# Optimization experiments

Measured on AMD Instinct MI355X. Metric: run time of the kernel, lower is better.

## Reference

```python
import jax, jax.numpy as jnp
import numpy as np
import math

NUM_IN_C = 128      # rep_2d num_c (c_z)
ATT_C = 64          # attention_num_c
NUM_HEADS = 4
B, T, I, J = 1, 4, 256, 256


def setup_inputs() -> dict:
    key = jax.random.key(0)
    ks = jax.random.split(key, 7)
    s = 1.0 / math.sqrt(NUM_IN_C)
    return {
        "z2d": jax.random.normal(ks[0], (B, I, J, NUM_IN_C), dtype=jnp.float32),
        "t2d": jax.random.normal(ks[1], (B, T, I, J, NUM_IN_C), dtype=jnp.float32),
        # nn.Linear weights are [out_features, in_features]; apply as x @ W.T
        "Wq": jax.random.normal(ks[2], (ATT_C * NUM_HEADS, NUM_IN_C), dtype=jnp.float32) * s,
        "Wk": jax.random.normal(ks[3], (ATT_C * NUM_HEADS, NUM_IN_C), dtype=jnp.float32) * s,
        "Wv": jax.random.normal(ks[4], (ATT_C * NUM_HEADS, NUM_IN_C), dtype=jnp.float32) * s,
        "Wo": jax.random.normal(ks[5], (NUM_IN_C, ATT_C * NUM_HEADS), dtype=jnp.float32) * s,
        "bo": jax.random.normal(ks[6], (NUM_IN_C,), dtype=jnp.float32) * 0.02,
    }


def reference(z2d, t2d, Wq, Wk, Wv, Wo, bo):
    # Projections; reshape last dim to (attention_num_c, num_heads) per torch .view
    q = (z2d @ Wq.T).reshape(*z2d.shape[:-1], ATT_C, NUM_HEADS)        # b i j c h
    k = (t2d @ Wk.T).reshape(*t2d.shape[:-1], ATT_C, NUM_HEADS)        # b t i j c h
    v = (t2d @ Wv.T).reshape(*t2d.shape[:-1], ATT_C, NUM_HEADS)        # b t i j c h
    # NOTE: original scales by sqrt(num_in_c), not sqrt(attention_num_c)
    scores = jnp.einsum('bijch,btijch->btijh', q, k) / math.sqrt(NUM_IN_C)
    w = jax.nn.softmax(scores, axis=1)                                  # softmax over template axis t
    out = jnp.einsum('btijh,btijch->bijch', w, v)                       # b i j c h
    out = out.reshape(*out.shape[:-2], ATT_C * NUM_HEADS)               # flatten (c,h)
    return out @ Wo.T + bo
```

## Files before the change

kernel.cpp:

```cpp
#include <hip/hip_runtime.h>


#define PIX 65536

typedef __attribute__((ext_vector_type(8))) short s8v;
typedef __attribute__((ext_vector_type(4))) float f4v;
typedef __attribute__((ext_vector_type(4))) unsigned int u4v;
typedef __attribute__((ext_vector_type(4))) float fl4;

__device__ __forceinline__ unsigned short f2bf(float x) {
    unsigned int u = __float_as_uint(x);
    u = (u + 0x7FFFu + ((u >> 16) & 1u)) >> 16;
    return (unsigned short)u;
}

__device__ __forceinline__ unsigned int cvtpk(float lo, float hi) {
    unsigned int r;
    asm("v_cvt_pk_bf16_f32 %0, %1, %2" : "=v"(r) : "v"(lo), "v"(hi));
    return r;
}

__device__ __forceinline__ s8v pack8(fl4 d0, fl4 d1) {
    union { u4v u; s8v s; } cv;
    cv.u[0] = cvtpk(d0[0], d0[1]);
    cv.u[1] = cvtpk(d0[2], d0[3]);
    cv.u[2] = cvtpk(d1[0], d1[1]);
    cv.u[3] = cvtpk(d1[2], d1[3]);
    return cv.s;
}

__device__ __forceinline__ float bflo(unsigned int u) { return __uint_as_float(u << 16); }
__device__ __forceinline__ float bfhi(unsigned int u) { return __uint_as_float(u & 0xffff0000u); }

__global__ __launch_bounds__(256) void build_weights(
        const float* __restrict__ Wq, const float* __restrict__ Wk,
        const float* __restrict__ Wv, const float* __restrict__ Wo,
        unsigned short* __restrict__ mcat, unsigned short* __restrict__ pcat) {
    int b = blockIdx.x;
    if (b < 256) {
        int idx = b * 256 + threadIdx.x;
        int n = idx >> 7, k1 = idx & 127;
        int h = n >> 7, k2 = n & 127;
        float s = 0.f;
        #pragma unroll 8
        for (int c = 0; c < 64; c++) {
            int r = c * 4 + h;
            s += Wq[r * 128 + k1] * Wk[r * 128 + k2];
        }
        mcat[idx] = f2bf(s * 0.088388347648318447f);
    } else {
        int idx = (b - 256) * 256 + threadIdx.x;
        int m = idx >> 9, kk = idx & 511;
        int h = kk >> 7, k = kk & 127;
        float s = 0.f;
        #pragma unroll 8
        for (int c = 0; c < 64; c++) {
            int r = c * 4 + h;
            s += Wo[m * 256 + r] * Wv[r * 128 + k];
        }
        pcat[idx] = f2bf(s);
    }
}

__global__ __launch_bounds__(256, 3) void score_kernel(
    const float* __restrict__ z2d, const float* __restrict__ t2d,
    const unsigned short* __restrict__ mcat, float* __restrict__ wbuf) {

    __shared__ unsigned short sm[128 * 128];
    const int tid = threadIdx.x;
    const int wv = tid >> 6, lane = tid & 63, quad = lane >> 4, l15 = lane & 15;
    const int p = blockIdx.x * 64 + wv * 16 + l15;

    s8v za[4];
    {
        const float* zp = z2d + (size_t)p * 128 + quad * 8;
        #pragma unroll
        for (int ks = 0; ks < 4; ks++)
            za[ks] = pack8(*(const fl4*)(zp + ks * 32), *(const fl4*)(zp + ks * 32 + 4));
    }
    unsigned int a2[4][8][2];
    #pragma unroll
    for (int t = 0; t < 4; t++) {
        const float* ap = t2d + ((size_t)t * PIX + p) * 128 + quad * 4;
        #pragma unroll
        for (int cb = 0; cb < 8; cb++) {
            const fl4 v = *(const fl4*)(ap + cb * 16);
            a2[t][cb][0] = cvtpk(v[0], v[1]);
            a2[t][cb][1] = cvtpk(v[2], v[3]);
        }
    }

    for (int h = 0; h < 4; h++) {
        __syncthreads();
        #pragma unroll
        for (int i = 0; i < 8; i++) {
            const int g8 = i * 256 + tid;
            const int row = g8 >> 4, c8 = g8 & 15;
            *(u4v*)&sm[row * 128 + ((c8 ^ (row & 7)) * 8)] =
                *(const u4v*)(mcat + (size_t)(h * 128 + row) * 128 + c8 * 8);
        }
        __syncthreads();

        float ps[4] = {0.f, 0.f, 0.f, 0.f};
        #pragma unroll
        for (int cb = 0; cb < 8; cb++) {
            f4v u = {0.f, 0.f, 0.f, 0.f};
            #pragma unroll
            for (int ks = 0; ks < 4; ks++) {
                const s8v a = *(const s8v*)&sm[(cb * 16 + l15) * 128 +
                                               (((ks * 4 + quad) ^ (l15 & 7)) * 8)];
                u = __builtin_amdgcn_mfma_f32_16x16x32_bf16(a, za[ks], u, 0, 0, 0);
            }
            #pragma unroll
            for (int t = 0; t < 4; t++) {
                const float a0 = bflo(a2[t][cb][0]), a1 = bfhi(a2[t][cb][0]);
                const float b0 = bflo(a2[t][cb][1]), b1 = bfhi(a2[t][cb][1]);
                ps[t] += u[0] * a0 + u[1] * a1 + u[2] * b0 + u[3] * b1;
            }
        }
        #pragma unroll
        for (int t = 0; t < 4; t++) {
            ps[t] += __shfl_xor(ps[t], 16);
            ps[t] += __shfl_xor(ps[t], 32);
        }
        const float mx = fmaxf(fmaxf(ps[0], ps[1]), fmaxf(ps[2], ps[3]));
        float e[4], sum = 0.f;
        #pragma unroll
        for (int t = 0; t < 4; t++) { e[t] = __expf(ps[t] - mx); sum += e[t]; }
        const float inv = 1.f / sum;
        if (quad == 0) {
            #pragma unroll
            for (int t = 0; t < 4; t++)
                wbuf[(size_t)(h * 4 + t) * PIX + p] = e[t] * inv;
        }
    }
}

__global__ __launch_bounds__(256, 3) void out_kernel(
    const float* __restrict__ t2d, const unsigned short* __restrict__ pcat,
    const float* __restrict__ wbuf, const float* __restrict__ bo,
    float* __restrict__ out) {

    __shared__ unsigned short sm[128 * 128];
    const int tid = threadIdx.x;
    const int wv = tid >> 6, lane = tid & 63, quad = lane >> 4, l15 = lane & 15;
    const int p0 = blockIdx.x * 64 + wv * 16;
    const int p = p0 + l15;

    float wgt[4][4];
    #pragma unroll
    for (int h = 0; h < 4; h++)
        #pragma unroll
        for (int t = 0; t < 4; t++)
            wgt[h][t] = wbuf[(size_t)(h * 4 + t) * PIX + p];

    s8v af[4][4];
    #pragma unroll
    for (int kf = 0; kf < 4; kf++) {
        float f[4][8];
        #pragma unroll
        for (int h = 0; h < 4; h++)
            #pragma unroll
            for (int j = 0; j < 8; j++) f[h][j] = 0.f;
        #pragma unroll
        for (int t = 0; t < 4; t++) {
            const float* ap = t2d + ((size_t)t * PIX + p) * 128 + kf * 32 + quad * 8;
            const fl4 d0 = *(const fl4*)ap;
            const fl4 d1 = *(const fl4*)(ap + 4);
            #pragma unroll
            for (int h = 0; h < 4; h++) {
                const float w = wgt[h][t];
                #pragma unroll
                for (int j = 0; j < 4; j++) {
                    f[h][j]     += w * d0[j];
                    f[h][j + 4] += w * d1[j];
                }
            }
        }
        #pragma unroll
        for (int h = 0; h < 4; h++) {
            union { u4v u; s8v s; } cv;
            cv.u[0] = cvtpk(f[h][0], f[h][1]);
            cv.u[1] = cvtpk(f[h][2], f[h][3]);
            cv.u[2] = cvtpk(f[h][4], f[h][5]);
            cv.u[3] = cvtpk(f[h][6], f[h][7]);
            af[h][kf] = cv.s;
        }
    }

    f4v acc[8];
    #pragma unroll
    for (int ct = 0; ct < 8; ct++) acc[ct] = (f4v){0.f, 0.f, 0.f, 0.f};

    for (int h = 0; h < 4; h++) {
        __syncthreads();
        #pragma unroll
        for (int i = 0; i < 8; i++) {
            const int g8 = i * 256 + tid;
            const int row = g8 >> 4, c8 = g8 & 15;
            *(u4v*)&sm[row * 128 + ((c8 ^ (row & 7)) * 8)] =
                *(const u4v*)(pcat + (size_t)row * 512 + h * 128 + c8 * 8);
        }
        __syncthreads();
        #pragma unroll
        for (int kf = 0; kf < 4; kf++)
            #pragma unroll
            for (int ct = 0; ct < 8; ct++) {
                const s8v b = *(const s8v*)&sm[(ct * 16 + l15) * 128 +
                                               (((kf * 4 + quad) ^ (l15 & 7)) * 8)];
                acc[ct] = __builtin_amdgcn_mfma_f32_16x16x32_bf16(af[h][kf], b, acc[ct], 0, 0, 0);
            }
    }

    #pragma unroll
    for (int ct = 0; ct < 8; ct++) {
        const float bb = bo[ct * 16 + l15];
        #pragma unroll
        for (int r = 0; r < 4; r++)
            out[(size_t)(p0 + quad * 4 + r) * 128 + ct * 16 + l15] = acc[ct][r] + bb;
    }
}

extern "C" void kernel_launch(void* const* d_in, const int* in_sizes, int n_in,
                              void* d_out, int out_size, void* d_ws, size_t ws_size,
                              hipStream_t stream) {
    const float* z2d = (const float*)d_in[0];
    const float* t2d = (const float*)d_in[1];
    const float* Wq  = (const float*)d_in[2];
    const float* Wk  = (const float*)d_in[3];
    const float* Wv  = (const float*)d_in[4];
    const float* Wo  = (const float*)d_in[5];
    const float* bo  = (const float*)d_in[6];

    unsigned short* mcat = (unsigned short*)d_ws;
    unsigned short* pcat = mcat + 512 * 128;
    float* wbuf = (float*)(pcat + 128 * 512);

    build_weights<<<512, 256, 0, stream>>>(Wq, Wk, Wv, Wo, mcat, pcat);
    score_kernel<<<1024, 256, 0, stream>>>(z2d, t2d, mcat, wbuf);
    out_kernel<<<1024, 256, 0, stream>>>(t2d, pcat, wbuf, bo, (float*)d_out);
}
```

Baseline: 312.3 us.

## Drop LDS staging of fused weights; read MFMA operands directly from global/L2

Both score and output kernels stop copying the fused bf16 weight matrices into shared memory and instead load MFMA operands straight from global memory, relying on L1/L2 caching. This removes the LDS fill, the barriers and the shared-memory footprint, which may raise occupancy. Blocks are halved to 128 threads (2048 blocks), and the output kernel now interleaves the weighted template reduction with MFMA accumulation instead of buffering all A fragments. The cost is many more uncoalesced-ish global loads per wave, which could stress the vector memory path and caches.

```diff
diff --git a/kernel.cpp b/kernel.cpp
--- a/kernel.cpp
+++ b/kernel.cpp
@@ -62,14 +62,13 @@
     }
 }
 
-__global__ __launch_bounds__(256, 3) void score_kernel(
+__global__ __launch_bounds__(128, 4) void score_kernel(
     const float* __restrict__ z2d, const float* __restrict__ t2d,
     const unsigned short* __restrict__ mcat, float* __restrict__ wbuf) {
 
-    __shared__ unsigned short sm[128 * 128];
     const int tid = threadIdx.x;
     const int wv = tid >> 6, lane = tid & 63, quad = lane >> 4, l15 = lane & 15;
-    const int p = blockIdx.x * 64 + wv * 16 + l15;
+    const int p = blockIdx.x * 32 + wv * 16 + l15;
 
     s8v za[4];
     {
@@ -91,31 +90,21 @@
     }
 
     for (int h = 0; h < 4; h++) {
-        __syncthreads();
-        #pragma unroll
-        for (int i = 0; i < 8; i++) {
-            const int g8 = i * 256 + tid;
-            const int row = g8 >> 4, c8 = g8 & 15;
-            *(u4v*)&sm[row * 128 + ((c8 ^ (row & 7)) * 8)] =
-                *(const u4v*)(mcat + (size_t)(h * 128 + row) * 128 + c8 * 8);
-        }
-        __syncthreads();
-
+        const unsigned short* mh = mcat + (size_t)h * 128 * 128;
         float ps[4] = {0.f, 0.f, 0.f, 0.f};
         #pragma unroll
         for (int cb = 0; cb < 8; cb++) {
             f4v u = {0.f, 0.f, 0.f, 0.f};
             #pragma unroll
             for (int ks = 0; ks < 4; ks++) {
-                const s8v a = *(const s8v*)&sm[(cb * 16 + l15) * 128 +
-                                               (((ks * 4 + quad) ^ (l15 & 7)) * 8)];
+                const s8v a = *(const s8v*)(mh + (size_t)(cb * 16 + l15) * 128
+                                            + ks * 32 + quad * 8);
                 u = __builtin_amdgcn_mfma_f32_16x16x32_bf16(a, za[ks], u, 0, 0, 0);
             }
             #pragma unroll
             for (int t = 0; t < 4; t++) {
-                const float a0 = bflo(a2[t][cb][0]), a1 = bfhi(a2[t][cb][0]);
-                const float b0 = bflo(a2[t][cb][1]), b1 = bfhi(a2[t][cb][1]);
-                ps[t] += u[0] * a0 + u[1] * a1 + u[2] * b0 + u[3] * b1;
+                ps[t] += u[0] * bflo(a2[t][cb][0]) + u[1] * bfhi(a2[t][cb][0])
+                       + u[2] * bflo(a2[t][cb][1]) + u[3] * bfhi(a2[t][cb][1]);
             }
         }
         #pragma unroll
@@ -136,15 +125,14 @@
     }
 }
 
-__global__ __launch_bounds__(256, 3) void out_kernel(
+__global__ __launch_bounds__(128, 4) void out_kernel(
     const float* __restrict__ t2d, const unsigned short* __restrict__ pcat,
     const float* __restrict__ wbuf, const float* __restrict__ bo,
     float* __restrict__ out) {
 
-    __shared__ unsigned short sm[128 * 128];
     const int tid = threadIdx.x;
     const int wv = tid >> 6, lane = tid & 63, quad = lane >> 4, l15 = lane & 15;
-    const int p0 = blockIdx.x * 64 + wv * 16;
+    const int p0 = blockIdx.x * 32 + wv * 16;
     const int p = p0 + l15;
 
     float wgt[4][4];
@@ -154,8 +142,10 @@
         for (int t = 0; t < 4; t++)
             wgt[h][t] = wbuf[(size_t)(h * 4 + t) * PIX + p];
 
-    s8v af[4][4];
-    #pragma unroll
+    f4v acc[8];
+    #pragma unroll
+    for (int ct = 0; ct < 8; ct++) acc[ct] = (f4v){0.f, 0.f, 0.f, 0.f};
+
     for (int kf = 0; kf < 4; kf++) {
         float f[4][8];
         #pragma unroll
@@ -184,32 +174,14 @@
             cv.u[1] = cvtpk(f[h][2], f[h][3]);
             cv.u[2] = cvtpk(f[h][4], f[h][5]);
             cv.u[3] = cvtpk(f[h][6], f[h][7]);
-            af[h][kf] = cv.s;
-        }
-    }
-
-    f4v acc[8];
-    #pragma unroll
-    for (int ct = 0; ct < 8; ct++) acc[ct] = (f4v){0.f, 0.f, 0.f, 0.f};
-
-    for (int h = 0; h < 4; h++) {
-        __syncthreads();
-        #pragma unroll
-        for (int i = 0; i < 8; i++) {
-            const int g8 = i * 256 + tid;
-            const int row = g8 >> 4, c8 = g8 & 15;
-            *(u4v*)&sm[row * 128 + ((c8 ^ (row & 7)) * 8)] =
-                *(const u4v*)(pcat + (size_t)row * 512 + h * 128 + c8 * 8);
-        }
-        __syncthreads();
-        #pragma unroll
-        for (int kf = 0; kf < 4; kf++)
+            const s8v af = cv.s;
             #pragma unroll
             for (int ct = 0; ct < 8; ct++) {
-                const s8v b = *(const s8v*)&sm[(ct * 16 + l15) * 128 +
-                                               (((kf * 4 + quad) ^ (l15 & 7)) * 8)];
-                acc[ct] = __builtin_amdgcn_mfma_f32_16x16x32_bf16(af[h][kf], b, acc[ct], 0, 0, 0);
-            }
+                const s8v b = *(const s8v*)(pcat + (size_t)(ct * 16 + l15) * 512
+                                            + h * 128 + kf * 32 + quad * 8);
+                acc[ct] = __builtin_amdgcn_mfma_f32_16x16x32_bf16(af, b, acc[ct], 0, 0, 0);
+            }
+        }
     }
 
     #pragma unroll
@@ -237,6 +209,6 @@
     float* wbuf = (float*)(pcat + 128 * 512);
 
     build_weights<<<512, 256, 0, stream>>>(Wq, Wk, Wv, Wo, mcat, pcat);
-    score_kernel<<<1024, 256, 0, stream>>>(z2d, t2d, mcat, wbuf);
-    out_kernel<<<1024, 256, 0, stream>>>(t2d, pcat, wbuf, bo, (float*)d_out);
-}
+    score_kernel<<<2048, 128, 0, stream>>>(z2d, t2d, mcat, wbuf);
+    out_kernel<<<2048, 128, 0, stream>>>(t2d, pcat, wbuf, bo, (float*)d_out);
+}
```

New measurement: 396.9 us. 1.27x slower.
